# Optimization experiments

Measured on AMD Instinct MI355X. Metric: run time of the kernel, lower is better.

## Reference

```python
import jax, jax.numpy as jnp
import numpy as np

B, S, D_IN, Z, D_OUT = 4, 2048, 4096, 1024, 4096
LN_EPS = 1e-5


def _ln(h, g, b):
    # LayerNorm over last axis (matches nn.LayerNorm(z_size))
    m = jnp.mean(h, axis=-1, keepdims=True)
    v = jnp.var(h, axis=-1, keepdims=True)
    return (h - m) * jax.lax.rsqrt(v + LN_EPS) * g + b


def setup_inputs() -> dict:
    key = jax.random.key(0)
    ks = jax.random.split(key, 8)
    s = 0.02  # init_weights uniform range
    return {
        "x": jax.random.normal(ks[0], (B, S, D_IN), jnp.float32),
        "epsilon": jax.random.normal(ks[1], (B, S, Z), jnp.float32),
        "W1": jax.random.uniform(ks[2], (Z, D_IN), jnp.float32, -s, s),
        "b1": jnp.zeros((Z,), jnp.float32),
        "g1": jnp.ones((Z,), jnp.float32),
        "be1": jnp.zeros((Z,), jnp.float32),
        "W2": jax.random.uniform(ks[3], (Z, Z), jnp.float32, -s, s),
        "b2": jnp.zeros((Z,), jnp.float32),
        "g2": jnp.ones((Z,), jnp.float32),
        "be2": jnp.zeros((Z,), jnp.float32),
        "Wmu": jax.random.uniform(ks[4], (Z, Z), jnp.float32, -s, s),
        "bmu": jnp.zeros((Z,), jnp.float32),
        "Wls": jax.random.uniform(ks[5], (Z, Z), jnp.float32, -s, s),
        "bls": jnp.zeros((Z,), jnp.float32),
        "Wzw": jax.random.uniform(ks[6], (D_OUT, D_OUT + Z), jnp.float32, -s, s),
        "bzw": jnp.zeros((D_OUT,), jnp.float32),
    }


def reference(x, epsilon, W1, b1, g1, be1, W2, b2, g2, be2,
              Wmu, bmu, Wls, bls, Wzw, bzw):
    # fc: Linear -> LayerNorm -> Tanh, twice
    h = jnp.tanh(_ln(jnp.einsum('bsd,zd->bsz', x, W1) + b1, g1, be1))
    h = jnp.tanh(_ln(jnp.einsum('bsz,yz->bsy', h, W2) + b2, g2, be2))
    mu = jnp.einsum('bsz,yz->bsy', h, Wmu) + bmu
    logsigma = jnp.einsum('bsz,yz->bsy', h, Wls) + bls
    std = jnp.exp(0.5 * logsigma)
    z = epsilon * std + mu                    # reparameterization
    z = jnp.concatenate([z, x], axis=2)       # [B,S,Z+D_IN]
    out = jnp.einsum('bsc,oc->bso', jnp.tanh(z), Wzw) + bzw
    return (out, mu, std)
```

## Files before the change

### kernel.cpp

```cpp
#include <hip/hip_runtime.h>
#include <cstdint>

typedef unsigned short u16;
typedef __bf16 bf16x8 __attribute__((ext_vector_type(8)));
typedef float f32x4 __attribute__((ext_vector_type(4)));

#define M_TOT 8192
#define D_IN  4096
#define Z_DIM 1024
#define D_OUT 4096
#define K_CAT 5120

struct alignas(8) u16x4 { u16 x, y, z, w; };

__device__ __forceinline__ u16 to_bf16(float f) {
    union { float f; uint32_t u; } v; v.f = f;
    uint32_t u = v.u;
    uint32_t r = (u + 0x7FFFu + ((u >> 16) & 1u)) >> 16;
    return (u16)r;
}

__device__ __forceinline__ void async_load16(const void* g, void* l) {
    __builtin_amdgcn_global_load_lds(
        (const __attribute__((address_space(1))) void*)g,
        (__attribute__((address_space(3))) void*)l,
        16, 0, 0);
}

__global__ __launch_bounds__(256)
void gemm_bt(const u16* __restrict__ A,
             const u16* __restrict__ Bw0, const u16* __restrict__ Bw1,
             const float* __restrict__ bias0, const float* __restrict__ bias1,
             float* __restrict__ C0, float* __restrict__ C1,
             int M, int N, int K)
{
    const u16*  Bw   = blockIdx.z ? Bw1   : Bw0;
    const float* bias = blockIdx.z ? bias1 : bias0;
    float*       C    = blockIdx.z ? C1    : C0;

    __shared__ u16 As[128 * 32];
    __shared__ u16 Bs[128 * 32];

    const int tid  = threadIdx.x;
    const int wave = tid >> 6;
    const int lane = tid & 63;
    const int m0 = blockIdx.y * 128;
    const int n0 = blockIdx.x * 128;
    const int wm = (wave & 1) * 64;
    const int wn = (wave >> 1) * 64;

    const int srow = wave * 32 + (lane >> 2);
    const int scol = (((lane & 3) ^ ((srow >> 1) & 3))) * 8;
    const long long a_off = (long long)(m0 + srow) * K + scol;
    const long long b_off = (long long)(n0 + srow) * K + scol;

    const int fr = lane & 15;
    const int fq = lane >> 4;
    const int rc = (fq ^ ((fr >> 1) & 3)) * 8;

    f32x4 acc[4][4] = {};

    for (int k0 = 0; k0 < K; k0 += 32) {
        async_load16(A  + a_off + k0,            &As[(wave * 32 +  0) * 32]);
        async_load16(A  + a_off + k0 + 16LL * K, &As[(wave * 32 + 16) * 32]);
        async_load16(Bw + b_off + k0,            &Bs[(wave * 32 +  0) * 32]);
        async_load16(Bw + b_off + k0 + 16LL * K, &Bs[(wave * 32 + 16) * 32]);
        __syncthreads();

        bf16x8 af[4], bf[4];
        #pragma unroll
        for (int i = 0; i < 4; i++)
            af[i] = *(const bf16x8*)&As[(wm + i * 16 + fr) * 32 + rc];
        #pragma unroll
        for (int i = 0; i < 4; i++)
            bf[i] = *(const bf16x8*)&Bs[(wn + i * 16 + fr) * 32 + rc];

        #pragma unroll
        for (int mi = 0; mi < 4; mi++)
            #pragma unroll
            for (int ni = 0; ni < 4; ni++)
                acc[mi][ni] = __builtin_amdgcn_mfma_f32_16x16x32_bf16(
                    af[mi], bf[ni], acc[mi][ni], 0, 0, 0);
        __syncthreads();
    }

    #pragma unroll
    for (int ni = 0; ni < 4; ni++) {
        const int col = n0 + wn + ni * 16 + fr;
        const float bv = bias[col];
        #pragma unroll
        for (int mi = 0; mi < 4; mi++) {
            const int row = m0 + wm + mi * 16 + fq * 4;
            float* cp = C + (long long)row * N + col;
            #pragma unroll
            for (int r = 0; r < 4; r++)
                cp[(long long)r * N] = acc[mi][ni][r] + bv;
        }
    }
}


#define BAR() do { asm volatile("" ::: "memory"); \
                   __builtin_amdgcn_s_barrier(); \
                   asm volatile("" ::: "memory"); } while (0)

#define STAGE_A(buf, h, kt_) do { if ((kt_) < nt) {                            \
    const u16* g_ = Ag + (long long)(h) * hstep + ((long long)(kt_) << 6);     \
    async_load16(g_,      &lds16[(buf) * 32768 + (h) * 8192        + wave * 512]); \
    async_load16(g_ + 32, &lds16[(buf) * 32768 + (h) * 8192 + 4096 + wave * 512]); \
  } } while (0)

#define STAGE_B(buf, h, kt_) do { if ((kt_) < nt) {                            \
    const u16* g_ = Bg + (long long)(h) * hstep + ((long long)(kt_) << 6);     \
    async_load16(g_,      &lds16[16384 + (buf) * 32768 + (h) * 8192        + wave * 512]); \
    async_load16(g_ + 32, &lds16[16384 + (buf) * 32768 + (h) * 8192 + 4096 + wave * 512]); \
  } } while (0)

#define LOAD_AF(buf, mbase)                                                    \
    _Pragma("unroll")                                                          \
    for (int mi_ = 0; mi_ < 4; ++mi_) {                                        \
      _Pragma("unroll")                                                        \
      for (int ks_ = 0; ks_ < 2; ++ks_)                                        \
        af[mi_][ks_] = *(const bf16x8*)&lds16[(buf) * 32768 + a_rd             \
                                              + ks_ * 4096 + ((mbase) + mi_) * 512]; \
    }

#define LOAD_B(dst, buf, nbase)                                                \
    _Pragma("unroll")                                                          \
    for (int ni_ = 0; ni_ < 2; ++ni_) {                                        \
      _Pragma("unroll")                                                        \
      for (int ks_ = 0; ks_ < 2; ++ks_)                                        \
        dst[ni_][ks_] = *(const bf16x8*)&lds16[(buf) * 32768 + b_rd            \
                                               + ks_ * 4096 + ((nbase) + ni_) * 512]; \
    }

#define MMA_Q(bfx, mo, no) do {                                                \
    __builtin_amdgcn_s_setprio(1);                                             \
    _Pragma("unroll")                                                          \
    for (int mi_ = 0; mi_ < 4; ++mi_) {                                        \
      _Pragma("unroll")                                                        \
      for (int ni_ = 0; ni_ < 2; ++ni_) {                                      \
        _Pragma("unroll")                                                      \
        for (int ks_ = 0; ks_ < 2; ++ks_)                                      \
          acc[(mo) + mi_][(no) + ni_] = __builtin_amdgcn_mfma_f32_16x16x32_bf16( \
              af[mi_][ks_], bfx[ni_][ks_], acc[(mo) + mi_][(no) + ni_], 0, 0, 0); \
      }                                                                        \
    }                                                                          \
    __builtin_amdgcn_s_setprio(0);                                             \
  } while (0)

#define TILE(b, kt_) do {                                                      \
             \
    LOAD_AF(b, 0);                                                             \
    STAGE_A((b) ^ 1, 0, (kt_) + 1);                                            \
    BAR();                                                                     \
    MMA_Q(bf0, 0, 0);                                                          \
    BAR();                                                                     \
                                            \
    LOAD_B(bf1, b, 2);                                                         \
    STAGE_A((b) ^ 1, 1, (kt_) + 1);                                            \
    BAR();                                                                     \
    MMA_Q(bf1, 0, 2);                                                          \
    BAR();                                                                     \
      \
    LOAD_AF(b, 4);                                                             \
    STAGE_B(b, 0, (kt_) + 2);                                                  \
    BAR();                                                                     \
    MMA_Q(bf0, 4, 0);                                                          \
    BAR();                                                                     \
              \
    STAGE_B(b, 1, (kt_) + 2);                                                  \
    if ((kt_) + 2 < nt) { asm volatile("s_waitcnt vmcnt(4)" ::: "memory"); }   \
    else                { asm volatile("s_waitcnt vmcnt(0)" ::: "memory"); }   \
    BAR();                                                                     \
    LOAD_B(bf0, (b) ^ 1, 0);                                                   \
    MMA_Q(bf1, 4, 2);                                                          \
    BAR();                                                                     \
  } while (0)

template <bool EXPLS>
__global__ __launch_bounds__(512)
void gemm256(const u16* __restrict__ A,
             const u16* __restrict__ Bw0, const u16* __restrict__ Bw1,
             const float* __restrict__ bias0, const float* __restrict__ bias1,
             float* __restrict__ C0, float* __restrict__ C1,
             int M, int N, int K)
{
    const u16*   Bw   = blockIdx.z ? Bw1   : Bw0;
    const float* bias = blockIdx.z ? bias1 : bias0;
    float*       C    = blockIdx.z ? C1    : C0;

    __shared__ u16 lds16[65536];

    const int tid  = threadIdx.x;
    const int wave = tid >> 6;
    const int lane = tid & 63;
    const int fr   = lane & 15;
    const int fq   = lane >> 4;
    const int wm   = (wave >> 2) * 128;
    const int wn   = (wave & 3) * 64;

    const int nwg  = (int)(gridDim.x * gridDim.y);
    const int bid0 = (int)(blockIdx.y * gridDim.x + blockIdx.x);
    const int bid  = (bid0 & 7) * (nwg >> 3) + (bid0 >> 3);
    const int n0   = (bid % (int)gridDim.x) * 256;
    const int m0   = (bid / (int)gridDim.x) * 256;

    const int nt = K >> 6;

    const int csrc = (tid & 3) ^ ((tid >> 4) & 2);
    const u16* Ag = A  + (long long)(m0 + (tid >> 2)) * K + csrc * 8;
    const u16* Bg = Bw + (long long)(n0 + (tid >> 2)) * K + csrc * 8;
    const long long hstep = 128LL * K;

    const int swz  = (fq * 8) ^ ((fr & 8) << 1);
    const int a_rd = (wave >> 2) * 8192 + fr * 32 + swz;
    const int b_rd = 16384 + ((wave & 3) >> 1) * 8192
                   + ((wave & 1) * 64 + fr) * 32 + swz;

    f32x4 acc[8][4] = {};
    bf16x8 af[4][2], bf0[2][2], bf1[2][2];

    STAGE_B(0, 0, 0);
    STAGE_B(0, 1, 0);
    STAGE_A(0, 0, 0);
    STAGE_A(0, 1, 0);
    STAGE_B(1, 0, 1);
    STAGE_B(1, 1, 1);
    asm volatile("s_waitcnt vmcnt(4)" ::: "memory");
    BAR();
    LOAD_B(bf0, 0, 0);

    #pragma unroll 1
    for (int kt = 0; kt < nt; kt += 2) {
        TILE(0, kt);
        TILE(1, kt + 1);
    }

    #pragma unroll
    for (int ni = 0; ni < 4; ++ni) {
        const int col = n0 + wn + ni * 16 + fr;
        const float bv = bias[col];
        #pragma unroll
        for (int mi = 0; mi < 8; ++mi) {
            const int row = m0 + wm + mi * 16 + fq * 4;
            float* cp = C + (long long)row * N + col;
            #pragma unroll
            for (int r = 0; r < 4; ++r) {
                float v = acc[mi][ni][r] + bv;
                if constexpr (EXPLS) { if (blockIdx.z) v = expf(0.5f * v); }
                cp[(long long)r * N] = v;
            }
        }
    }
}

#undef BAR
#undef STAGE_A
#undef STAGE_B
#undef LOAD_AF
#undef LOAD_B
#undef MMA_Q
#undef TILE

__global__ __launch_bounds__(256)
void ln_tanh_kernel(const float* __restrict__ in, const float* __restrict__ g,
                    const float* __restrict__ be, u16* __restrict__ out)
{
    const int row = blockIdx.x;
    const int t = threadIdx.x;
    const float4 v = ((const float4*)(in + (long long)row * 1024))[t];
    float s  = v.x + v.y + v.z + v.w;
    float s2 = v.x * v.x + v.y * v.y + v.z * v.z + v.w * v.w;
    #pragma unroll
    for (int off = 32; off > 0; off >>= 1) {
        s  += __shfl_down(s,  off);
        s2 += __shfl_down(s2, off);
    }
    __shared__ float red[8];
    if ((t & 63) == 0) { red[t >> 6] = s; red[4 + (t >> 6)] = s2; }
    __syncthreads();
    s  = red[0] + red[1] + red[2] + red[3];
    s2 = red[4] + red[5] + red[6] + red[7];
    const float mean = s * (1.0f / 1024.0f);
    const float inv  = rsqrtf(s2 * (1.0f / 1024.0f) - mean * mean + 1e-5f);
    const float4 gg = ((const float4*)g)[t];
    const float4 bb = ((const float4*)be)[t];
    u16x4 o;
    o.x = to_bf16(tanhf((v.x - mean) * inv * gg.x + bb.x));
    o.y = to_bf16(tanhf((v.y - mean) * inv * gg.y + bb.y));
    o.z = to_bf16(tanhf((v.z - mean) * inv * gg.z + bb.z));
    o.w = to_bf16(tanhf((v.w - mean) * inv * gg.w + bb.w));
    ((u16x4*)(out + (long long)row * 1024))[t] = o;
}

__global__ __launch_bounds__(256)
void prep_x_kernel(const float* __restrict__ x, u16* __restrict__ xb,
                   u16* __restrict__ zc)
{
    const long long i = (long long)blockIdx.x * 256 + threadIdx.x;
    const float4 v = ((const float4*)x)[i];
    u16x4 b;
    b.x = to_bf16(v.x); b.y = to_bf16(v.y); b.z = to_bf16(v.z); b.w = to_bf16(v.w);
    ((u16x4*)xb)[i] = b;
    const long long flat = i * 4;
    const long long row = flat >> 12;
    const int col = (int)(flat & 4095);
    u16x4 tq;
    tq.x = to_bf16(tanhf(v.x)); tq.y = to_bf16(tanhf(v.y));
    tq.z = to_bf16(tanhf(v.z)); tq.w = to_bf16(tanhf(v.w));
    *(u16x4*)(zc + row * (long long)K_CAT + 1024 + col) = tq;
}

__global__ __launch_bounds__(256)
void reparam_kernel(const float* __restrict__ mu, const float* __restrict__ stdv,
                    const float* __restrict__ eps, u16* __restrict__ zc)
{
    const long long row = blockIdx.x;
    const int c = threadIdx.x * 4;
    const long long idx = row * 1024 + c;
    const float4 m = *(const float4*)(mu + idx);
    const float4 sd = *(const float4*)(stdv + idx);
    const float4 e = *(const float4*)(eps + idx);
    u16x4 t;
    t.x = to_bf16(tanhf(e.x * sd.x + m.x));
    t.y = to_bf16(tanhf(e.y * sd.y + m.y));
    t.z = to_bf16(tanhf(e.z * sd.z + m.z));
    t.w = to_bf16(tanhf(e.w * sd.w + m.w));
    *(u16x4*)(zc + row * (long long)K_CAT + c) = t;
}

__global__ __launch_bounds__(256)
void cvt_kernel(const float* __restrict__ src, u16* __restrict__ dst, long long n4)
{
    const long long i = (long long)blockIdx.x * 256 + threadIdx.x;
    if (i >= n4) return;
    const float4 v = ((const float4*)src)[i];
    u16x4 b;
    b.x = to_bf16(v.x); b.y = to_bf16(v.y); b.z = to_bf16(v.z); b.w = to_bf16(v.w);
    ((u16x4*)dst)[i] = b;
}

__global__ __launch_bounds__(256)
void cvt4_kernel(const float* __restrict__ s0, u16* __restrict__ d0,
                 const float* __restrict__ s1, u16* __restrict__ d1,
                 const float* __restrict__ s2, u16* __restrict__ d2,
                 const float* __restrict__ s3, u16* __restrict__ d3)
{
    long long i = (long long)blockIdx.x * 256 + threadIdx.x;
    const float* s; u16* d;
    if (i < 1048576)      { s = s0; d = d0; }
    else if (i < 1310720) { s = s1; d = d1; i -= 1048576; }
    else if (i < 1572864) { s = s2; d = d2; i -= 1310720; }
    else                  { s = s3; d = d3; i -= 1572864; }
    const float4 v = ((const float4*)s)[i];
    u16x4 b;
    b.x = to_bf16(v.x); b.y = to_bf16(v.y); b.z = to_bf16(v.z); b.w = to_bf16(v.w);
    ((u16x4*)d)[i] = b;
}

extern "C" void kernel_launch(void* const* d_in, const int* in_sizes, int n_in,
                              void* d_out, int out_size, void* d_ws, size_t ws_size,
                              hipStream_t stream)
{
    const float* x   = (const float*)d_in[0];
    const float* eps = (const float*)d_in[1];
    const float* W1  = (const float*)d_in[2];
    const float* b1  = (const float*)d_in[3];
    const float* g1  = (const float*)d_in[4];
    const float* be1 = (const float*)d_in[5];
    const float* W2  = (const float*)d_in[6];
    const float* b2  = (const float*)d_in[7];
    const float* g2  = (const float*)d_in[8];
    const float* be2 = (const float*)d_in[9];
    const float* Wmu = (const float*)d_in[10];
    const float* bmu = (const float*)d_in[11];
    const float* Wls = (const float*)d_in[12];
    const float* bls = (const float*)d_in[13];
    const float* Wzw = (const float*)d_in[14];
    const float* bzw = (const float*)d_in[15];

    float* out  = (float*)d_out;
    float* mu   = out + (long long)M_TOT * D_OUT;
    float* std_ = mu  + (long long)M_TOT * Z_DIM;

    char* ws = (char*)d_ws;
    u16*   xb   = (u16*)(ws);
    u16*   zc   = (u16*)(ws +  67108864);
    u16*   h1   = (u16*)(ws + 150994944);
    u16*   h2   = (u16*)(ws + 167772160);
    float* pre  = (float*)(ws + 184549376);
    u16*   W1b  = (u16*)(ws + 218103808);
    u16*   W2b  = (u16*)(ws + 226492416);
    u16*   Wmub = (u16*)(ws + 228589568);
    u16*   Wlsb = (u16*)(ws + 230686720);
    u16*   Wzwb = (u16*)(ws);

    cvt4_kernel<<<7168, 256, 0, stream>>>(W1, W1b, W2, W2b, Wmu, Wmub, Wls, Wlsb);

    prep_x_kernel<<<32768, 256, 0, stream>>>(x, xb, zc);

    gemm_bt<<<dim3(8, 64, 1), 256, 0, stream>>>(xb, W1b, W1b, b1, b1, pre, pre,
                                                M_TOT, Z_DIM, D_IN);
    ln_tanh_kernel<<<8192, 256, 0, stream>>>(pre, g1, be1, h1);

    cvt_kernel<<<20480, 256, 0, stream>>>(Wzw, Wzwb, 5242880);

    gemm_bt<<<dim3(8, 64, 1), 256, 0, stream>>>(h1, W2b, W2b, b2, b2, pre, pre,
                                                M_TOT, Z_DIM, Z_DIM);
    ln_tanh_kernel<<<8192, 256, 0, stream>>>(pre, g2, be2, h2);

    gemm256<true><<<dim3(4, 32, 2), 512, 0, stream>>>(h2, Wmub, Wlsb, bmu, bls,
                                                      mu, std_,
                                                      M_TOT, Z_DIM, Z_DIM);

    reparam_kernel<<<8192, 256, 0, stream>>>(mu, std_, eps, zc);

    gemm256<false><<<dim3(16, 32, 1), 512, 0, stream>>>(zc, Wzwb, Wzwb, bzw, bzw,
                                                        out, out,
                                                        M_TOT, D_OUT, K_CAT);
}
```

Measured before the change: 906.1 us.

## Replace simple 128x128 GEMM with pipelined 256x128 GEMM for FC layers

Replaces the single-buffered 128x128-tile gemm_bt, which synchronises twice per 32-wide K step, with a new gemm128n kernel. The new kernel uses 256x128 tiles, 512 threads and a 64-wide K step. It double-buffers A and B in LDS with async global-to-LDS loads, prefetches B fragments one tile ahead, and remaps block IDs for L2 locality. The aim is to hide global load latency behind MFMA work for the two Z-output GEMMs. The cost is larger LDS use (96KB) and fewer blocks (256) on a device with many CUs, which may leave some CUs idle.

```diff
diff --git a/kernel.cpp b/kernel.cpp
--- a/kernel.cpp
+++ b/kernel.cpp
@@ -27,82 +27,10 @@
         16, 0, 0);
 }
 
-__global__ __launch_bounds__(256)
-void gemm_bt(const u16* __restrict__ A,
-             const u16* __restrict__ Bw0, const u16* __restrict__ Bw1,
-             const float* __restrict__ bias0, const float* __restrict__ bias1,
-             float* __restrict__ C0, float* __restrict__ C1,
-             int M, int N, int K)
-{
-    const u16*  Bw   = blockIdx.z ? Bw1   : Bw0;
-    const float* bias = blockIdx.z ? bias1 : bias0;
-    float*       C    = blockIdx.z ? C1    : C0;
-
-    __shared__ u16 As[128 * 32];
-    __shared__ u16 Bs[128 * 32];
-
-    const int tid  = threadIdx.x;
-    const int wave = tid >> 6;
-    const int lane = tid & 63;
-    const int m0 = blockIdx.y * 128;
-    const int n0 = blockIdx.x * 128;
-    const int wm = (wave & 1) * 64;
-    const int wn = (wave >> 1) * 64;
-
-    const int srow = wave * 32 + (lane >> 2);
-    const int scol = (((lane & 3) ^ ((srow >> 1) & 3))) * 8;
-    const long long a_off = (long long)(m0 + srow) * K + scol;
-    const long long b_off = (long long)(n0 + srow) * K + scol;
-
-    const int fr = lane & 15;
-    const int fq = lane >> 4;
-    const int rc = (fq ^ ((fr >> 1) & 3)) * 8;
-
-    f32x4 acc[4][4] = {};
-
-    for (int k0 = 0; k0 < K; k0 += 32) {
-        async_load16(A  + a_off + k0,            &As[(wave * 32 +  0) * 32]);
-        async_load16(A  + a_off + k0 + 16LL * K, &As[(wave * 32 + 16) * 32]);
-        async_load16(Bw + b_off + k0,            &Bs[(wave * 32 +  0) * 32]);
-        async_load16(Bw + b_off + k0 + 16LL * K, &Bs[(wave * 32 + 16) * 32]);
-        __syncthreads();
-
-        bf16x8 af[4], bf[4];
-        #pragma unroll
-        for (int i = 0; i < 4; i++)
-            af[i] = *(const bf16x8*)&As[(wm + i * 16 + fr) * 32 + rc];
-        #pragma unroll
-        for (int i = 0; i < 4; i++)
-            bf[i] = *(const bf16x8*)&Bs[(wn + i * 16 + fr) * 32 + rc];
-
-        #pragma unroll
-        for (int mi = 0; mi < 4; mi++)
-            #pragma unroll
-            for (int ni = 0; ni < 4; ni++)
-                acc[mi][ni] = __builtin_amdgcn_mfma_f32_16x16x32_bf16(
-                    af[mi], bf[ni], acc[mi][ni], 0, 0, 0);
-        __syncthreads();
-    }
-
-    #pragma unroll
-    for (int ni = 0; ni < 4; ni++) {
-        const int col = n0 + wn + ni * 16 + fr;
-        const float bv = bias[col];
-        #pragma unroll
-        for (int mi = 0; mi < 4; mi++) {
-            const int row = m0 + wm + mi * 16 + fq * 4;
-            float* cp = C + (long long)row * N + col;
-            #pragma unroll
-            for (int r = 0; r < 4; r++)
-                cp[(long long)r * N] = acc[mi][ni][r] + bv;
-        }
-    }
-}
-
-
 #define BAR() do { asm volatile("" ::: "memory"); \
                    __builtin_amdgcn_s_barrier(); \
                    asm volatile("" ::: "memory"); } while (0)
+
 
 #define STAGE_A(buf, h, kt_) do { if ((kt_) < nt) {                            \
     const u16* g_ = Ag + (long long)(h) * hstep + ((long long)(kt_) << 6);     \
@@ -150,25 +78,21 @@
   } while (0)
 
 #define TILE(b, kt_) do {                                                      \
-             \
     LOAD_AF(b, 0);                                                             \
     STAGE_A((b) ^ 1, 0, (kt_) + 1);                                            \
     BAR();                                                                     \
     MMA_Q(bf0, 0, 0);                                                          \
     BAR();                                                                     \
-                                            \
     LOAD_B(bf1, b, 2);                                                         \
     STAGE_A((b) ^ 1, 1, (kt_) + 1);                                            \
     BAR();                                                                     \
     MMA_Q(bf1, 0, 2);                                                          \
     BAR();                                                                     \
-      \
     LOAD_AF(b, 4);                                                             \
     STAGE_B(b, 0, (kt_) + 2);                                                  \
     BAR();                                                                     \
     MMA_Q(bf0, 4, 0);                                                          \
     BAR();                                                                     \
-              \
     STAGE_B(b, 1, (kt_) + 2);                                                  \
     if ((kt_) + 2 < nt) { asm volatile("s_waitcnt vmcnt(4)" ::: "memory"); }   \
     else                { asm volatile("s_waitcnt vmcnt(0)" ::: "memory"); }   \
@@ -255,13 +179,148 @@
     }
 }
 
-#undef BAR
 #undef STAGE_A
 #undef STAGE_B
 #undef LOAD_AF
 #undef LOAD_B
 #undef MMA_Q
 #undef TILE
+
+
+#define STAGE_A1(buf, h, kt_) do { if ((kt_) < nt) {                           \
+    const u16* g_ = Ag + (long long)(h) * hstep + ((long long)(kt_) << 6);     \
+    async_load16(g_,      &lds16[(buf) * 24576 + (h) * 8192        + wave * 512]); \
+    async_load16(g_ + 32, &lds16[(buf) * 24576 + (h) * 8192 + 4096 + wave * 512]); \
+  } } while (0)
+
+#define STAGE_B1(buf, kt_) do { if ((kt_) < nt) {                              \
+    const u16* g_ = Bg + ((long long)(kt_) << 6);                              \
+    async_load16(g_,      &lds16[(buf) * 24576 + 16384        + wave * 512]);  \
+    async_load16(g_ + 32, &lds16[(buf) * 24576 + 16384 + 4096 + wave * 512]);  \
+  } } while (0)
+
+#define LOAD_AF1(buf, mbase)                                                   \
+    _Pragma("unroll")                                                          \
+    for (int mi_ = 0; mi_ < 4; ++mi_) {                                        \
+      _Pragma("unroll")                                                        \
+      for (int ks_ = 0; ks_ < 2; ++ks_)                                        \
+        af[mi_][ks_] = *(const bf16x8*)&lds16[(buf) * 24576 + a_rd             \
+                                              + ks_ * 4096 + ((mbase) + mi_) * 512]; \
+    }
+
+#define LOAD_BF1(dst, buf)                                                     \
+    _Pragma("unroll")                                                          \
+    for (int ni_ = 0; ni_ < 2; ++ni_) {                                        \
+      _Pragma("unroll")                                                        \
+      for (int ks_ = 0; ks_ < 2; ++ks_)                                        \
+        dst[ni_][ks_] = *(const bf16x8*)&lds16[(buf) * 24576 + b_rd            \
+                                               + ks_ * 4096 + ni_ * 512];      \
+    }
+
+#define MMA_H(bfx, mo) do {                                                    \
+    __builtin_amdgcn_s_setprio(1);                                             \
+    _Pragma("unroll")                                                          \
+    for (int mi_ = 0; mi_ < 4; ++mi_) {                                        \
+      _Pragma("unroll")                                                        \
+      for (int ni_ = 0; ni_ < 2; ++ni_) {                                      \
+        _Pragma("unroll")                                                      \
+        for (int ks_ = 0; ks_ < 2; ++ks_)                                      \
+          acc[(mo) + mi_][ni_] = __builtin_amdgcn_mfma_f32_16x16x32_bf16(      \
+              af[mi_][ks_], bfx[ni_][ks_], acc[(mo) + mi_][ni_], 0, 0, 0);     \
+      }                                                                        \
+    }                                                                          \
+    __builtin_amdgcn_s_setprio(0);                                             \
+  } while (0)
+
+#define TILE1(b, kt_, bfCur, bfNxt) do {                                       \
+                                     \
+    LOAD_AF1(b, 0);                                                            \
+    STAGE_A1((b) ^ 1, 0, (kt_) + 1);                                           \
+    BAR();                                                                     \
+    MMA_H(bfCur, 0);                                                           \
+    BAR();                                                                     \
+         \
+    LOAD_AF1(b, 4);                                                            \
+    STAGE_A1((b) ^ 1, 1, (kt_) + 1);                                           \
+    STAGE_B1(b, (kt_) + 2);                                                    \
+    if ((kt_) + 2 < nt) { asm volatile("s_waitcnt vmcnt(2)" ::: "memory"); }   \
+    else                { asm volatile("s_waitcnt vmcnt(0)" ::: "memory"); }   \
+    BAR();                                                                     \
+    LOAD_BF1(bfNxt, (b) ^ 1);                                                  \
+    MMA_H(bfCur, 4);                                                           \
+    BAR();                                                                     \
+  } while (0)
+
+__global__ __launch_bounds__(512)
+void gemm128n(const u16* __restrict__ A, const u16* __restrict__ Bw,
+              const float* __restrict__ bias, float* __restrict__ C,
+              int M, int N, int K)
+{
+    __shared__ u16 lds16[49152];
+
+    const int tid  = threadIdx.x;
+    const int wave = tid >> 6;
+    const int lane = tid & 63;
+    const int fr   = lane & 15;
+    const int fq   = lane >> 4;
+    const int wm   = (wave >> 2) * 128;
+    const int wn   = (wave & 3) * 32;
+
+    const int nwg  = (int)(gridDim.x * gridDim.y);
+    const int bid0 = (int)(blockIdx.y * gridDim.x + blockIdx.x);
+    const int bid  = (bid0 & 7) * (nwg >> 3) + (bid0 >> 3);
+    const int n0   = (bid % (int)gridDim.x) * 128;
+    const int m0   = (bid / (int)gridDim.x) * 256;
+
+    const int nt = K >> 6;
+
+    const int csrc = (tid & 3) ^ ((tid >> 4) & 2);
+    const u16* Ag = A  + (long long)(m0 + (tid >> 2)) * K + csrc * 8;
+    const u16* Bg = Bw + (long long)(n0 + (tid >> 2)) * K + csrc * 8;
+    const long long hstep = 128LL * K;
+
+    const int swz  = (fq * 8) ^ ((fr & 8) << 1);
+    const int a_rd = (wave >> 2) * 8192 + fr * 32 + swz;
+    const int b_rd = 16384 + ((wave & 3) * 32 + fr) * 32 + swz;
+
+    f32x4 acc[8][2] = {};
+    bf16x8 af[4][2], bfA[2][2], bfB[2][2];
+
+    STAGE_B1(0, 0);
+    STAGE_A1(0, 0, 0);
+    STAGE_A1(0, 1, 0);
+    STAGE_B1(1, 1);
+    asm volatile("s_waitcnt vmcnt(2)" ::: "memory");
+    BAR();
+    LOAD_BF1(bfA, 0);
+
+    #pragma unroll 1
+    for (int kt = 0; kt < nt; kt += 2) {
+        TILE1(0, kt,     bfA, bfB);
+        TILE1(1, kt + 1, bfB, bfA);
+    }
+
+    #pragma unroll
+    for (int ni = 0; ni < 2; ++ni) {
+        const int col = n0 + wn + ni * 16 + fr;
+        const float bv = bias[col];
+        #pragma unroll
+        for (int mi = 0; mi < 8; ++mi) {
+            const int row = m0 + wm + mi * 16 + fq * 4;
+            float* cp = C + (long long)row * N + col;
+            #pragma unroll
+            for (int r = 0; r < 4; ++r)
+                cp[(long long)r * N] = acc[mi][ni][r] + bv;
+        }
+    }
+}
+
+#undef STAGE_A1
+#undef STAGE_B1
+#undef LOAD_AF1
+#undef LOAD_BF1
+#undef MMA_H
+#undef TILE1
 
 __global__ __launch_bounds__(256)
 void ln_tanh_kernel(const float* __restrict__ in, const float* __restrict__ g,
@@ -400,14 +459,14 @@
 
     prep_x_kernel<<<32768, 256, 0, stream>>>(x, xb, zc);
 
-    gemm_bt<<<dim3(8, 64, 1), 256, 0, stream>>>(xb, W1b, W1b, b1, b1, pre, pre,
-                                                M_TOT, Z_DIM, D_IN);
+    gemm128n<<<dim3(8, 32, 1), 512, 0, stream>>>(xb, W1b, b1, pre,
+                                                 M_TOT, Z_DIM, D_IN);
     ln_tanh_kernel<<<8192, 256, 0, stream>>>(pre, g1, be1, h1);
 
     cvt_kernel<<<20480, 256, 0, stream>>>(Wzw, Wzwb, 5242880);
 
-    gemm_bt<<<dim3(8, 64, 1), 256, 0, stream>>>(h1, W2b, W2b, b2, b2, pre, pre,
-                                                M_TOT, Z_DIM, Z_DIM);
+    gemm128n<<<dim3(8, 32, 1), 512, 0, stream>>>(h1, W2b, b2, pre,
+                                                 M_TOT, Z_DIM, Z_DIM);
     ln_tanh_kernel<<<8192, 256, 0, stream>>>(pre, g2, be2, h2);
 
     gemm256<true><<<dim3(4, 32, 2), 512, 0, stream>>>(h2, Wmub, Wlsb, bmu, bls,
```

New measurement: 877.2 us. 3.2% less time.
